# Performance work log

Hardware: AMD Instinct MI355X
Metric: run time of the kernel (lower is better)

## Reference

```python
import jax, jax.numpy as jnp
import numpy as np

NUM_VIEWS = 11

def setup_inputs() -> dict:
    key = jax.random.key(0)
    ks = jax.random.split(key, 6)
    BF, T, D_IN, D_OUT, R = 128, 196, 1024, 1024, 4
    B = 16
    x = jax.random.normal(ks[0], (BF, T, D_IN), dtype=jnp.float32)
    view_idx = jax.random.randint(ks[1], (B,), 0, NUM_VIEWS)
    W = jax.random.normal(ks[2], (D_OUT, D_IN), dtype=jnp.float32) * (1.0 / np.sqrt(D_IN))
    b = jax.random.normal(ks[3], (D_OUT,), dtype=jnp.float32) * 0.01
    lora_A = jax.random.normal(ks[4], (NUM_VIEWS, D_IN, R), dtype=jnp.float32) * (1.0 / np.sqrt(D_IN))
    lora_B = jax.random.normal(ks[5], (NUM_VIEWS, R, D_OUT), dtype=jnp.float32) * 0.02
    return {"x": x, "view_idx": view_idx, "W": W, "b": b, "lora_A": lora_A, "lora_B": lora_B}

def reference(x, view_idx, W, b, lora_A, lora_B):
    # base linear: [BF, T, D_in] @ [D_in, D_out]
    out = jnp.einsum('bti,oi->bto', x, W) + b
    BF = x.shape[0]
    B = view_idx.shape[0]
    if BF != B:  # static shapes -> Python branch is jit-safe
        curr = jnp.repeat(view_idx, BF // B)  # expand per-frame view index
    else:
        curr = view_idx
    curr = jnp.clip(curr, 0, NUM_VIEWS - 1)
    A = lora_A[curr]          # [BF, D_in, R] gathered per sample
    Bm = lora_B[curr]         # [BF, R, D_out]
    h = jnp.einsum('bti,bir->btr', x, A)      # low-rank projection
    lora = jnp.einsum('btr,bro->bto', h, Bm)  # back to D_out
    return out + lora
```

## Files before the change

kernel.cpp:

```cpp
#include <hip/hip_runtime.h>
#include <hip/hip_bf16.h>
#include <stdint.h>

#define M_TOT 25088
#define N_TOT 1024
#define K_TOT 1024
#define T_LEN 196
#define NVIEW 11
#define ROWS_PER_VIEW 1568

#define BM 128
#define BN 128
#define BK 64

typedef unsigned short u16;
typedef __bf16 bf16x8 __attribute__((ext_vector_type(8)));
typedef float f32x4 __attribute__((ext_vector_type(4)));
typedef unsigned short u16x8 __attribute__((ext_vector_type(8)));

#define XB_ELEMS ((size_t)M_TOT * K_TOT)
#define WB_ELEMS ((size_t)N_TOT * K_TOT)
#define WB_OFF_B (XB_ELEMS * 2)
#define H_OFF_B  (WB_OFF_B + WB_ELEMS * 2)
#define WS_NEEDED (H_OFF_B + (size_t)M_TOT * 4 * 4)

__device__ __forceinline__ u16 f2bf(float f) {
    union { float f; unsigned int i; } c; c.f = f;
    unsigned int i = c.i;
    return (u16)((i + 0x7FFFu + ((i >> 16) & 1u)) >> 16);
}
__device__ __forceinline__ float bf2f(unsigned int u) {
    union { unsigned int i; float f; } c; c.i = u << 16; return c.f;
}

__global__ __launch_bounds__(256) void cast_kernel(
    const float* __restrict__ x, const float* __restrict__ W,
    u16* __restrict__ xb, u16* __restrict__ wb) {
    const size_t e = ((size_t)blockIdx.x * 256 + threadIdx.x) * 8;
    const float* src;
    u16* dst;
    if (e < XB_ELEMS) { src = x + e; dst = xb + e; }
    else              { src = W + (e - XB_ELEMS); dst = wb + (e - XB_ELEMS); }
    float4 v0 = *(const float4*)src;
    float4 v1 = *(const float4*)(src + 4);
    u16x8 o = { f2bf(v0.x), f2bf(v0.y), f2bf(v0.z), f2bf(v0.w),
                f2bf(v1.x), f2bf(v1.y), f2bf(v1.z), f2bf(v1.w) };
    *(u16x8*)dst = o;
}

__global__ __launch_bounds__(256) void h_kernel(
    const u16* __restrict__ xb, const int* __restrict__ view_idx,
    const float* __restrict__ lora_A, float* __restrict__ h) {
    const int row  = blockIdx.x * 4 + (threadIdx.x >> 6);
    const int lane = threadIdx.x & 63;
    int v = view_idx[row / ROWS_PER_VIEW];
    v = v < 0 ? 0 : (v > NVIEW - 1 ? NVIEW - 1 : v);
    const float* A = lora_A + (size_t)v * (K_TOT * 4);
    const unsigned int* xr = (const unsigned int*)(xb + (size_t)row * K_TOT);

    float a0 = 0.f, a1 = 0.f, a2 = 0.f, a3 = 0.f;
#pragma unroll
    for (int it = 0; it < 8; ++it) {
        unsigned int p = xr[it * 64 + lane];
        float x0 = bf2f(p & 0xffffu);
        float x1 = bf2f(p >> 16);
        const int k = it * 128 + lane * 2;
        float4 av0 = *(const float4*)(A + (size_t)k * 4);
        float4 av1 = *(const float4*)(A + (size_t)k * 4 + 4);
        a0 += x0 * av0.x + x1 * av1.x;
        a1 += x0 * av0.y + x1 * av1.y;
        a2 += x0 * av0.z + x1 * av1.z;
        a3 += x0 * av0.w + x1 * av1.w;
    }
#pragma unroll
    for (int off = 32; off > 0; off >>= 1) {
        a0 += __shfl_xor(a0, off, 64);
        a1 += __shfl_xor(a1, off, 64);
        a2 += __shfl_xor(a2, off, 64);
        a3 += __shfl_xor(a3, off, 64);
    }
    if (lane == 0)
        *(float4*)(h + (size_t)row * 4) = make_float4(a0, a1, a2, a3);
}

__global__ __launch_bounds__(256) void h_only_kernel(
    const float* __restrict__ x, const int* __restrict__ view_idx,
    const float* __restrict__ lora_A, float* __restrict__ h) {
    const int row  = blockIdx.x * 4 + (threadIdx.x >> 6);
    const int lane = threadIdx.x & 63;
    int v = view_idx[row / ROWS_PER_VIEW];
    v = v < 0 ? 0 : (v > NVIEW - 1 ? NVIEW - 1 : v);
    const float* A  = lora_A + (size_t)v * (K_TOT * 4);
    const float* xr = x + (size_t)row * K_TOT;
    float a0 = 0.f, a1 = 0.f, a2 = 0.f, a3 = 0.f;
#pragma unroll
    for (int it = 0; it < 16; ++it) {
        const int k = it * 64 + lane;
        float xf = xr[k];
        float4 av = *(const float4*)(A + (size_t)k * 4);
        a0 += xf * av.x; a1 += xf * av.y; a2 += xf * av.z; a3 += xf * av.w;
    }
#pragma unroll
    for (int off = 32; off > 0; off >>= 1) {
        a0 += __shfl_xor(a0, off, 64);
        a1 += __shfl_xor(a1, off, 64);
        a2 += __shfl_xor(a2, off, 64);
        a3 += __shfl_xor(a3, off, 64);
    }
    if (lane == 0)
        *(float4*)(h + (size_t)row * 4) = make_float4(a0, a1, a2, a3);
}

template <bool CONV>
__global__ __launch_bounds__(256) void gemm_lora_kernel(
    const void* __restrict__ xp, const void* __restrict__ Wp,
    const float* __restrict__ bias, const int* __restrict__ view_idx,
    const float* __restrict__ lora_B, const float* __restrict__ h,
    float* __restrict__ out) {
    __shared__ u16 As[BM * BK];
    __shared__ u16 Bs[BN * BK];

    const int tid = threadIdx.x;
    const int id = blockIdx.x;
    int bx, by;
    if (id < 1536) { const int c = id >> 6, w = id & 63; by = c * 8 + (w & 7); bx = w >> 3; }
    else           { const int r = id - 1536; by = 192 + (r & 3); bx = r >> 2; }

    const int lane = tid & 63;
    const int wave = tid >> 6;
    const int wm   = (wave >> 1) * 64;
    const int wn   = (wave & 1) * 64;
    const int l16  = lane & 15;
    const int quad = lane >> 4;

    const size_t a_base = (size_t)(by * BM) * K_TOT;
    const size_t b_base = (size_t)(bx * BN) * K_TOT;

    f32x4 acc[4][4] = {};

    for (int kt = 0; kt < K_TOT / BK; ++kt) {
        const int kofs = kt * BK;
        if constexpr (!CONV) {
            const u16* x = (const u16*)xp;
            const u16* W = (const u16*)Wp;
#pragma unroll
            for (int i = 0; i < 4; ++i) {
                const int e = i * 2048 + tid * 8;
                const int r = e >> 6, c = e & 63;
                __builtin_amdgcn_global_load_lds(
                    (const __attribute__((address_space(1))) void*)(x + a_base + (size_t)r * K_TOT + kofs + c),
                    (__attribute__((address_space(3))) void*)(As + e), 16, 0, 0);
                __builtin_amdgcn_global_load_lds(
                    (const __attribute__((address_space(1))) void*)(W + b_base + (size_t)r * K_TOT + kofs + c),
                    (__attribute__((address_space(3))) void*)(Bs + e), 16, 0, 0);
            }
        } else {
            const float* x = (const float*)xp;
            const float* W = (const float*)Wp;
#pragma unroll
            for (int i = 0; i < 8; ++i) {
                const int e = i * 1024 + tid * 4;
                const int r = e >> 6, c = e & 63;
                float4 av = *(const float4*)(x + a_base + (size_t)r * K_TOT + kofs + c);
                float4 bv = *(const float4*)(W + b_base + (size_t)r * K_TOT + kofs + c);
                *(u16*)(As + e)     = f2bf(av.x); *(u16*)(As + e + 1) = f2bf(av.y);
                *(u16*)(As + e + 2) = f2bf(av.z); *(u16*)(As + e + 3) = f2bf(av.w);
                *(u16*)(Bs + e)     = f2bf(bv.x); *(u16*)(Bs + e + 1) = f2bf(bv.y);
                *(u16*)(Bs + e + 2) = f2bf(bv.z); *(u16*)(Bs + e + 3) = f2bf(bv.w);
            }
        }
        __syncthreads();
#pragma unroll
        for (int kk = 0; kk < 2; ++kk) {
            const int k0 = kk * 32 + quad * 8;
            bf16x8 a_frag[4], b_frag[4];
#pragma unroll
            for (int mi = 0; mi < 4; ++mi)
                a_frag[mi] = *(const bf16x8*)(const void*)(As + (wm + mi * 16 + l16) * BK + k0);
#pragma unroll
            for (int ni = 0; ni < 4; ++ni)
                b_frag[ni] = *(const bf16x8*)(const void*)(Bs + (wn + ni * 16 + l16) * BK + k0);
#pragma unroll
            for (int mi = 0; mi < 4; ++mi)
#pragma unroll
                for (int ni = 0; ni < 4; ++ni)
                    acc[mi][ni] = __builtin_amdgcn_mfma_f32_16x16x32_bf16(
                        a_frag[mi], b_frag[ni], acc[mi][ni], 0, 0, 0);
        }
        __syncthreads();
    }

    const int rowBase = by * BM + wm;
    const int colBase = bx * BN + wn;
    float biasv[4];
#pragma unroll
    for (int ni = 0; ni < 4; ++ni) biasv[ni] = bias[colBase + ni * 16 + l16];

    const int ve0 = (by * BM) / ROWS_PER_VIEW;
    const int ve1 = (by * BM + BM - 1) / ROWS_PER_VIEW;
    if (ve0 == ve1) {
        int v = view_idx[ve0];
        v = v < 0 ? 0 : (v > NVIEW - 1 ? NVIEW - 1 : v);
        const float* Bv = lora_B + (size_t)v * (4 * N_TOT);
        float Bvv[4][4];
#pragma unroll
        for (int r = 0; r < 4; ++r)
#pragma unroll
            for (int ni = 0; ni < 4; ++ni)
                Bvv[r][ni] = Bv[r * N_TOT + colBase + ni * 16 + l16];
#pragma unroll
        for (int mi = 0; mi < 4; ++mi) {
#pragma unroll
            for (int reg = 0; reg < 4; ++reg) {
                const int grow = rowBase + mi * 16 + quad * 4 + reg;
                const float4 hv = *(const float4*)(h + (size_t)grow * 4);
                float* orow = out + (size_t)grow * N_TOT;
#pragma unroll
                for (int ni = 0; ni < 4; ++ni) {
                    float lora = hv.x * Bvv[0][ni] + hv.y * Bvv[1][ni]
                               + hv.z * Bvv[2][ni] + hv.w * Bvv[3][ni];
                    orow[colBase + ni * 16 + l16] = acc[mi][ni][reg] + biasv[ni] + lora;
                }
            }
        }
    } else {
#pragma unroll
        for (int mi = 0; mi < 4; ++mi) {
#pragma unroll
            for (int reg = 0; reg < 4; ++reg) {
                const int grow = rowBase + mi * 16 + quad * 4 + reg;
                int v = view_idx[grow / ROWS_PER_VIEW];
                v = v < 0 ? 0 : (v > NVIEW - 1 ? NVIEW - 1 : v);
                const float4 hv = *(const float4*)(h + (size_t)grow * 4);
                const float* Bv = lora_B + (size_t)v * (4 * N_TOT);
                float* orow = out + (size_t)grow * N_TOT;
#pragma unroll
                for (int ni = 0; ni < 4; ++ni) {
                    const int gcol = colBase + ni * 16 + l16;
                    float lora = hv.x * Bv[gcol]
                               + hv.y * Bv[N_TOT + gcol]
                               + hv.z * Bv[2 * N_TOT + gcol]
                               + hv.w * Bv[3 * N_TOT + gcol];
                    orow[gcol] = acc[mi][ni][reg] + biasv[ni] + lora;
                }
            }
        }
    }
}

extern "C" void kernel_launch(void* const* d_in, const int* in_sizes, int n_in,
                              void* d_out, int out_size, void* d_ws, size_t ws_size,
                              hipStream_t stream) {
    const float* x        = (const float*)d_in[0];
    const int*   view_idx = (const int*)d_in[1];
    const float* W        = (const float*)d_in[2];
    const float* b        = (const float*)d_in[3];
    const float* lora_A   = (const float*)d_in[4];
    const float* lora_B   = (const float*)d_in[5];
    float* out = (float*)d_out;

    const dim3 ggrid((M_TOT / BM) * (N_TOT / BN));
    if (ws_size >= WS_NEEDED) {
        u16*   xb = (u16*)d_ws;
        u16*   wb = (u16*)((char*)d_ws + WB_OFF_B);
        float* h  = (float*)((char*)d_ws + H_OFF_B);
        const int cast_blocks = (int)((XB_ELEMS + WB_ELEMS) / (8 * 256));
        hipLaunchKernelGGL(cast_kernel, dim3(cast_blocks), dim3(256), 0, stream, x, W, xb, wb);
        hipLaunchKernelGGL(h_kernel, dim3(M_TOT / 4), dim3(256), 0, stream, xb, view_idx, lora_A, h);
        hipLaunchKernelGGL((gemm_lora_kernel<false>), ggrid, dim3(256), 0, stream,
                           xb, wb, b, view_idx, lora_B, h, out);
    } else {
        float* h = (float*)d_ws;
        hipLaunchKernelGGL(h_only_kernel, dim3(M_TOT / 4), dim3(256), 0, stream,
                           x, view_idx, lora_A, h);
        hipLaunchKernelGGL((gemm_lora_kernel<true>), ggrid, dim3(256), 0, stream,
                           x, W, b, view_idx, lora_B, h, out);
    }
}
```

Baseline: 304.4 us.

## Fuse cast and LoRA-down into one prep kernel; XOR-swizzle GEMM LDS tiles

```diff
diff --git a/kernel.cpp b/kernel.cpp
--- a/kernel.cpp
+++ b/kernel.cpp
@@ -16,7 +16,7 @@
 typedef unsigned short u16;
 typedef __bf16 bf16x8 __attribute__((ext_vector_type(8)));
 typedef float f32x4 __attribute__((ext_vector_type(4)));
-typedef unsigned short u16x8 __attribute__((ext_vector_type(8)));
+typedef unsigned short u16x4 __attribute__((ext_vector_type(4)));
 
 #define XB_ELEMS ((size_t)M_TOT * K_TOT)
 #define WB_ELEMS ((size_t)N_TOT * K_TOT)
@@ -29,48 +29,54 @@
     unsigned int i = c.i;
     return (u16)((i + 0x7FFFu + ((i >> 16) & 1u)) >> 16);
 }
-__device__ __forceinline__ float bf2f(unsigned int u) {
-    union { unsigned int i; float f; } c; c.i = u << 16; return c.f;
-}
-
-__global__ __launch_bounds__(256) void cast_kernel(
+
+__global__ __launch_bounds__(256) void prep_kernel(
     const float* __restrict__ x, const float* __restrict__ W,
-    u16* __restrict__ xb, u16* __restrict__ wb) {
-    const size_t e = ((size_t)blockIdx.x * 256 + threadIdx.x) * 8;
-    const float* src;
-    u16* dst;
-    if (e < XB_ELEMS) { src = x + e; dst = xb + e; }
-    else              { src = W + (e - XB_ELEMS); dst = wb + (e - XB_ELEMS); }
-    float4 v0 = *(const float4*)src;
-    float4 v1 = *(const float4*)(src + 4);
-    u16x8 o = { f2bf(v0.x), f2bf(v0.y), f2bf(v0.z), f2bf(v0.w),
-                f2bf(v1.x), f2bf(v1.y), f2bf(v1.z), f2bf(v1.w) };
-    *(u16x8*)dst = o;
-}
-
-__global__ __launch_bounds__(256) void h_kernel(
-    const u16* __restrict__ xb, const int* __restrict__ view_idx,
-    const float* __restrict__ lora_A, float* __restrict__ h) {
-    const int row  = blockIdx.x * 4 + (threadIdx.x >> 6);
+    const int* __restrict__ view_idx, const float* __restrict__ lora_A,
+    u16* __restrict__ xb, u16* __restrict__ wb, float* __restrict__ h) {
+    const int wave = threadIdx.x >> 6;
     const int lane = threadIdx.x & 63;
+    const int blk  = blockIdx.x;
+
+    if (blk >= M_TOT / 4) {
+        const int row = (blk - M_TOT / 4) * 4 + wave;
+        const float* src = W + (size_t)row * K_TOT;
+        u16* dst = wb + (size_t)row * K_TOT;
+#pragma unroll
+        for (int it = 0; it < 4; ++it) {
+            const int k = it * 256 + lane * 4;
+            float4 v = *(const float4*)(src + k);
+            u16x4 o = { f2bf(v.x), f2bf(v.y), f2bf(v.z), f2bf(v.w) };
+            *(u16x4*)(dst + k) = o;
+        }
+        return;
+    }
+
+    const int row = blk * 4 + wave;
     int v = view_idx[row / ROWS_PER_VIEW];
     v = v < 0 ? 0 : (v > NVIEW - 1 ? NVIEW - 1 : v);
-    const float* A = lora_A + (size_t)v * (K_TOT * 4);
-    const unsigned int* xr = (const unsigned int*)(xb + (size_t)row * K_TOT);
-
+    const float* A  = lora_A + (size_t)v * (K_TOT * 4);
+    const float* xr = x + (size_t)row * K_TOT;
+    u16* dst = xb + (size_t)row * K_TOT;
+
+#pragma unroll
+    for (int it = 0; it < 4; ++it) {
+        const int k = it * 256 + lane * 4;
+        float4 xv = *(const float4*)(xr + k);
+        u16x4 o = { f2bf(xv.x), f2bf(xv.y), f2bf(xv.z), f2bf(xv.w) };
+        *(u16x4*)(dst + k) = o;
+    }
     float a0 = 0.f, a1 = 0.f, a2 = 0.f, a3 = 0.f;
 #pragma unroll
     for (int it = 0; it < 8; ++it) {
-        unsigned int p = xr[it * 64 + lane];
-        float x0 = bf2f(p & 0xffffu);
-        float x1 = bf2f(p >> 16);
         const int k = it * 128 + lane * 2;
+        float2 xv = *(const float2*)(xr + k);
         float4 av0 = *(const float4*)(A + (size_t)k * 4);
         float4 av1 = *(const float4*)(A + (size_t)k * 4 + 4);
-        a0 += x0 * av0.x + x1 * av1.x;
-        a1 += x0 * av0.y + x1 * av1.y;
-        a2 += x0 * av0.z + x1 * av1.z;
-        a3 += x0 * av0.w + x1 * av1.w;
+        a0 += xv.x * av0.x + xv.y * av1.x;
+        a1 += xv.x * av0.y + xv.y * av1.y;
+        a2 += xv.x * av0.z + xv.y * av1.z;
+        a3 += xv.x * av0.w + xv.y * av1.w;
     }
 #pragma unroll
     for (int off = 32; off > 0; off >>= 1) {
@@ -94,11 +100,15 @@
     const float* xr = x + (size_t)row * K_TOT;
     float a0 = 0.f, a1 = 0.f, a2 = 0.f, a3 = 0.f;
 #pragma unroll
-    for (int it = 0; it < 16; ++it) {
-        const int k = it * 64 + lane;
-        float xf = xr[k];
-        float4 av = *(const float4*)(A + (size_t)k * 4);
-        a0 += xf * av.x; a1 += xf * av.y; a2 += xf * av.z; a3 += xf * av.w;
+    for (int it = 0; it < 8; ++it) {
+        const int k = it * 128 + lane * 2;
+        float2 xv = *(const float2*)(xr + k);
+        float4 av0 = *(const float4*)(A + (size_t)k * 4);
+        float4 av1 = *(const float4*)(A + (size_t)k * 4 + 4);
+        a0 += xv.x * av0.x + xv.y * av1.x;
+        a1 += xv.x * av0.y + xv.y * av1.y;
+        a2 += xv.x * av0.z + xv.y * av1.z;
+        a3 += xv.x * av0.w + xv.y * av1.w;
     }
 #pragma unroll
     for (int off = 32; off > 0; off >>= 1) {
@@ -132,6 +142,7 @@
     const int wn   = (wave & 1) * 64;
     const int l16  = lane & 15;
     const int quad = lane >> 4;
+    const int sw   = l16 & 7;
 
     const size_t a_base = (size_t)(by * BM) * K_TOT;
     const size_t b_base = (size_t)(bx * BN) * K_TOT;
@@ -146,7 +157,8 @@
 #pragma unroll
             for (int i = 0; i < 4; ++i) {
                 const int e = i * 2048 + tid * 8;
-                const int r = e >> 6, c = e & 63;
+                const int r = e >> 6;
+                const int c = (((tid & 7) ^ (r & 7)) << 3);
                 __builtin_amdgcn_global_load_lds(
                     (const __attribute__((address_space(1))) void*)(x + a_base + (size_t)r * K_TOT + kofs + c),
                     (__attribute__((address_space(3))) void*)(As + e), 16, 0, 0);
@@ -160,26 +172,27 @@
 #pragma unroll
             for (int i = 0; i < 8; ++i) {
                 const int e = i * 1024 + tid * 4;
-                const int r = e >> 6, c = e & 63;
-                float4 av = *(const float4*)(x + a_base + (size_t)r * K_TOT + kofs + c);
-                float4 bv = *(const float4*)(W + b_base + (size_t)r * K_TOT + kofs + c);
-                *(u16*)(As + e)     = f2bf(av.x); *(u16*)(As + e + 1) = f2bf(av.y);
-                *(u16*)(As + e + 2) = f2bf(av.z); *(u16*)(As + e + 3) = f2bf(av.w);
-                *(u16*)(Bs + e)     = f2bf(bv.x); *(u16*)(Bs + e + 1) = f2bf(bv.y);
-                *(u16*)(Bs + e + 2) = f2bf(bv.z); *(u16*)(Bs + e + 3) = f2bf(bv.w);
+                const int r = e >> 6, o = e & 63;
+                const int d = r * 64 + (((o >> 3) ^ (r & 7)) << 3) + (o & 7);
+                float4 av = *(const float4*)(x + a_base + (size_t)r * K_TOT + kofs + o);
+                float4 bv = *(const float4*)(W + b_base + (size_t)r * K_TOT + kofs + o);
+                u16x4 ao = { f2bf(av.x), f2bf(av.y), f2bf(av.z), f2bf(av.w) };
+                u16x4 bo = { f2bf(bv.x), f2bf(bv.y), f2bf(bv.z), f2bf(bv.w) };
+                *(u16x4*)(As + d) = ao;
+                *(u16x4*)(Bs + d) = bo;
             }
         }
         __syncthreads();
 #pragma unroll
         for (int kk = 0; kk < 2; ++kk) {
-            const int k0 = kk * 32 + quad * 8;
+            const int csw = (((kk * 4 + quad) ^ sw) << 3);
             bf16x8 a_frag[4], b_frag[4];
 #pragma unroll
             for (int mi = 0; mi < 4; ++mi)
-                a_frag[mi] = *(const bf16x8*)(const void*)(As + (wm + mi * 16 + l16) * BK + k0);
+                a_frag[mi] = *(const bf16x8*)(const void*)(As + (wm + mi * 16 + l16) * BK + csw);
 #pragma unroll
             for (int ni = 0; ni < 4; ++ni)
-                b_frag[ni] = *(const bf16x8*)(const void*)(Bs + (wn + ni * 16 + l16) * BK + k0);
+                b_frag[ni] = *(const bf16x8*)(const void*)(Bs + (wn + ni * 16 + l16) * BK + csw);
 #pragma unroll
             for (int mi = 0; mi < 4; ++mi)
 #pragma unroll
@@ -264,9 +277,8 @@
         u16*   xb = (u16*)d_ws;
         u16*   wb = (u16*)((char*)d_ws + WB_OFF_B);
         float* h  = (float*)((char*)d_ws + H_OFF_B);
-        const int cast_blocks = (int)((XB_ELEMS + WB_ELEMS) / (8 * 256));
-        hipLaunchKernelGGL(cast_kernel, dim3(cast_blocks), dim3(256), 0, stream, x, W, xb, wb);
-        hipLaunchKernelGGL(h_kernel, dim3(M_TOT / 4), dim3(256), 0, stream, xb, view_idx, lora_A, h);
+        hipLaunchKernelGGL(prep_kernel, dim3(M_TOT / 4 + N_TOT / 4), dim3(256), 0, stream,
+                           x, W, view_idx, lora_A, xb, wb, h);
         hipLaunchKernelGGL((gemm_lora_kernel<false>), ggrid, dim3(256), 0, stream,
                            xb, wb, b, view_idx, lora_B, h, out);
     } else {
```

New measurement: 275.9 us. 1.1x faster.
